# Performance work log

Hardware: AMD Instinct MI355X
Metric: run time of the kernel (lower is better)

Reference implementation:

```python
import jax, jax.numpy as jnp
import numpy as np

N_A, N_B = 30000, 30000
V, D_IN, D_OUT, H, E = 2, 128, 128, 4, 480000
EPS_LN = 1e-5


def setup_inputs() -> dict:
    key = jax.random.key(0)
    ks = jax.random.split(key, 22)
    rn = lambda i, sh, s=1.0: jax.random.normal(ks[i], sh, dtype=jnp.float32) * s
    ri = lambda i, n: jax.random.randint(ks[i], (E,), 0, n, dtype=jnp.int32)
    return {
        'feat_A': rn(0, (N_A, V, D_IN)),
        'feat_B': rn(1, (N_B, V, D_IN)),
        'src_ab': ri(2, N_A), 'dst_ab': ri(3, N_B),
        'val_ab': jax.random.uniform(ks[4], (E,), dtype=jnp.float32),
        'src_ba': ri(5, N_B), 'dst_ba': ri(6, N_A),
        'val_ba': jax.random.uniform(ks[7], (E,), dtype=jnp.float32),
        'W1': rn(8, (D_OUT, D_IN), 0.05), 'b1': jnp.zeros((D_OUT,), jnp.float32),
        'g1': jnp.ones((D_OUT,), jnp.float32), 'be1': jnp.zeros((D_OUT,), jnp.float32),
        'W2': rn(9, (D_OUT, D_IN), 0.05), 'b2': jnp.zeros((D_OUT,), jnp.float32),
        'g2': jnp.ones((D_OUT,), jnp.float32), 'be2': jnp.zeros((D_OUT,), jnp.float32),
        'Win': rn(10, (3 * D_OUT, D_OUT), 0.05), 'bin_': jnp.zeros((3 * D_OUT,), jnp.float32),
        'Wout': rn(11, (D_OUT, D_OUT), 0.05), 'bout': jnp.zeros((D_OUT,), jnp.float32),
        'lng': jnp.ones((D_OUT,), jnp.float32), 'lnb': jnp.zeros((D_OUT,), jnp.float32),
    }


def spmm_t(src, dst, val, h, n_out):
    # (adj^T @ h) over all views: h [N_src, V, d] -> [n_out, V, d]
    msg = h[src] * val[:, None, None]
    return jax.ops.segment_sum(msg, dst, num_segments=n_out)


def l2norm(x):
    n = jnp.sqrt(jnp.sum(x * x, axis=-1, keepdims=True))
    return x / jnp.maximum(n, 1e-12)


def layernorm(x, g, b):
    mu = jnp.mean(x, axis=-1, keepdims=True)
    var = jnp.mean((x - mu) ** 2, axis=-1, keepdims=True)
    return (x - mu) * jax.lax.rsqrt(var + EPS_LN) * g + b


def proj(x, W, b, g, be):
    # Linear -> LayerNorm -> ReLU
    return jax.nn.relu(layernorm(x @ W.T + b, g, be))


def mha(x, Win, bin_, Wout, bout, num_heads):
    # self-attention over the metapath axis P; x [..., P, d]
    *lead, P, d = x.shape
    dh = d // num_heads
    q, k, v = jnp.split(x @ Win.T + bin_, 3, axis=-1)
    hd = lambda t: t.reshape(*lead, P, num_heads, dh)
    q = hd(q) * (dh ** -0.5)
    scores = jnp.einsum('...qhe,...khe->...hqk', q, hd(k))
    a = jax.nn.softmax(scores, axis=-1)
    o = jnp.einsum('...hqk,...khe->...qhe', a, hd(v)).reshape(*lead, P, d)
    return o @ Wout.T + bout


def reference(feat_A, feat_B, src_ab, dst_ab, val_ab, src_ba, dst_ba, val_ba,
              W1, b1, g1, be1, W2, b2, g2, be2, Win, bin_, Wout, bout, lng, lnb):
    # metapath A->B->A
    h = l2norm(spmm_t(src_ab, dst_ab, val_ab, feat_A, N_B))
    h = l2norm(spmm_t(src_ba, dst_ba, val_ba, h, N_A))
    h1 = proj(h, W1, b1, g1, be1)                       # [N_A, V, d]
    # metapath B->A
    h = l2norm(spmm_t(src_ba, dst_ba, val_ba, feat_B, N_A))
    h2 = proj(h, W2, b2, g2, be2)                       # [N_A, V, d]
    x = jnp.stack([h1, h2], axis=2)                     # [N_A, V, P=2, d]
    attn = mha(x, Win, bin_, Wout, bout, H)
    y = layernorm(attn + x, lng, lnb).mean(axis=2)      # [N_A, V, d]
    return y  # h_global['A']; type B is identity passthrough of feat_B
```

## Files before the change

kernel.cpp:

```cpp
#include <hip/hip_runtime.h>

#define D 128
#define NODE_ROW 256
#define AP 8
#define AR (AP * 2)

typedef __attribute__((ext_vector_type(8))) short short8;
typedef __attribute__((ext_vector_type(4))) float floatx4;

__device__ __forceinline__ ushort f2bf(float f) {
    unsigned int u = __float_as_uint(f);
    u += 0x7fffu + ((u >> 16) & 1u);
    return (ushort)(u >> 16);
}
__device__ __forceinline__ unsigned int pk2(float a, float b) {
    return (unsigned int)f2bf(a) | ((unsigned int)f2bf(b) << 16);
}
__device__ __forceinline__ void up8(uint4 u, float* f) {
    f[0] = __uint_as_float(u.x << 16); f[1] = __uint_as_float(u.x & 0xffff0000u);
    f[2] = __uint_as_float(u.y << 16); f[3] = __uint_as_float(u.y & 0xffff0000u);
    f[4] = __uint_as_float(u.z << 16); f[5] = __uint_as_float(u.z & 0xffff0000u);
    f[6] = __uint_as_float(u.w << 16); f[7] = __uint_as_float(u.w & 0xffff0000u);
}
__device__ __forceinline__ float bf2f(ushort h) {
    return __uint_as_float(((unsigned int)h) << 16);
}
__device__ __forceinline__ short8 ldfrag(const ushort* p) {
    union { uint4 u; short8 s; } cv;
    cv.u = *(const uint4*)p;
    return cv.s;
}
__device__ __forceinline__ void acc4(float4& a, float w, uint2 u) {
    a.x += w * __uint_as_float(u.x << 16);
    a.y += w * __uint_as_float(u.x & 0xffff0000u);
    a.z += w * __uint_as_float(u.y << 16);
    a.w += w * __uint_as_float(u.y & 0xffff0000u);
}

__global__ __launch_bounds__(256) void k_f2b2(
    const float* __restrict__ srcA, const float* __restrict__ srcB,
    ushort* __restrict__ dstA, ushort* __restrict__ dstB, int n8) {
    int i = blockIdx.x * 256 + threadIdx.x;
    const float* s; ushort* d; int k;
    if (i < n8) { s = srcA; d = dstA; k = i; }
    else if (i < 2 * n8) { s = srcB; d = dstB; k = i - n8; }
    else return;
    const float4* sp = (const float4*)s + (size_t)k * 2;
    float4 a = sp[0], b = sp[1];
    uint4 o;
    o.x = pk2(a.x, a.y); o.y = pk2(a.z, a.w);
    o.z = pk2(b.x, b.y); o.w = pk2(b.z, b.w);
    ((uint4*)d)[k] = o;
}


__global__ __launch_bounds__(256) void k_hist(
    const int* __restrict__ dst_ab, const int* __restrict__ dst_ba,
    int* __restrict__ cnt_ab, int* __restrict__ cnt_ba, int E) {
    int i = blockIdx.x * 256 + threadIdx.x;
    if (i >= E) return;
    atomicAdd(&cnt_ab[dst_ab[i]], 1);
    atomicAdd(&cnt_ba[dst_ba[i]], 1);
}

__global__ __launch_bounds__(1024) void k_scan(
    const int* __restrict__ cnt, int* __restrict__ start, int n) {
    __shared__ int part[1024];
    int t = threadIdx.x;
    int chunk = (n + 1023) >> 10;
    int lo = min(t * chunk, n), hi = min(lo + chunk, n);
    int s = 0;
    for (int i = lo; i < hi; i++) s += cnt[i];
    part[t] = s;
    __syncthreads();
    for (int d = 1; d < 1024; d <<= 1) {
        int v = (t >= d) ? part[t - d] : 0;
        __syncthreads();
        part[t] += v;
        __syncthreads();
    }
    int off = part[t] - s;
    for (int i = lo; i < hi; i++) { start[i] = off; off += cnt[i]; }
    if (t == 1023) start[n] = off;
}

__global__ __launch_bounds__(256) void k_scatter(
    const int* __restrict__ src_ab, const int* __restrict__ dst_ab,
    const float* __restrict__ val_ab,
    const int* __restrict__ src_ba, const int* __restrict__ dst_ba,
    const float* __restrict__ val_ba,
    const int* __restrict__ start_ab, const int* __restrict__ start_ba,
    int* __restrict__ cnt_ab, int* __restrict__ cnt_ba,
    int2* __restrict__ ep_ab, int2* __restrict__ ep_ba, int E) {
    int i = blockIdx.x * 256 + threadIdx.x;
    if (i >= E) return;
    {
        int dd = dst_ab[i];
        int pos = start_ab[dd] + atomicAdd(&cnt_ab[dd], 1);
        ep_ab[pos] = make_int2(src_ab[i], __float_as_int(val_ab[i]));
    }
    {
        int dd = dst_ba[i];
        int pos = start_ba[dd] + atomicAdd(&cnt_ba[dd], 1);
        ep_ba[pos] = make_int2(src_ba[i], __float_as_int(val_ba[i]));
    }
}


__global__ __launch_bounds__(256) void k_gather_norm_bf(
    const ushort* __restrict__ feat, const int2* __restrict__ ep,
    const int* __restrict__ start, ushort* __restrict__ out, int n) {
    int node = blockIdx.x * 4 + (threadIdx.x >> 6);
    if (node >= n) return;
    int lane = threadIdx.x & 63;
    int lo = start[node], hi = start[node + 1];
    float4 acc = make_float4(0.f, 0.f, 0.f, 0.f);
    int i = lo;
    for (; i + 3 < hi; i += 4) {
        int2 p0 = ep[i], p1 = ep[i + 1], p2 = ep[i + 2], p3 = ep[i + 3];
        uint2 u0 = ((const uint2*)(feat + (size_t)p0.x * NODE_ROW))[lane];
        uint2 u1 = ((const uint2*)(feat + (size_t)p1.x * NODE_ROW))[lane];
        uint2 u2 = ((const uint2*)(feat + (size_t)p2.x * NODE_ROW))[lane];
        uint2 u3 = ((const uint2*)(feat + (size_t)p3.x * NODE_ROW))[lane];
        acc4(acc, __int_as_float(p0.y), u0);
        acc4(acc, __int_as_float(p1.y), u1);
        acc4(acc, __int_as_float(p2.y), u2);
        acc4(acc, __int_as_float(p3.y), u3);
    }
    for (; i < hi; i++) {
        int2 p = ep[i];
        uint2 u = ((const uint2*)(feat + (size_t)p.x * NODE_ROW))[lane];
        acc4(acc, __int_as_float(p.y), u);
    }
    float ss = acc.x * acc.x + acc.y * acc.y + acc.z * acc.z + acc.w * acc.w;
    #pragma unroll
    for (int o = 16; o > 0; o >>= 1) ss += __shfl_xor(ss, o, 32);
    float sc = 1.0f / fmaxf(sqrtf(ss), 1e-12f);
    uint2 o;
    o.x = pk2(acc.x * sc, acc.y * sc);
    o.y = pk2(acc.z * sc, acc.w * sc);
    ((uint2*)(out + (size_t)node * NODE_ROW))[lane] = o;
}

__global__ __launch_bounds__(256) void k_gather2_bf(
    const ushort* __restrict__ featP, const ushort* __restrict__ featQ,
    const int2* __restrict__ ep, const int* __restrict__ start,
    ushort* __restrict__ outP, ushort* __restrict__ outQ, int n) {
    int node = blockIdx.x * 4 + (threadIdx.x >> 6);
    if (node >= n) return;
    int lane = threadIdx.x & 63;
    int lo = start[node], hi = start[node + 1];
    float4 aP = make_float4(0.f, 0.f, 0.f, 0.f);
    float4 aQ = make_float4(0.f, 0.f, 0.f, 0.f);
    int i = lo;
    for (; i + 3 < hi; i += 4) {
        int2 p0 = ep[i], p1 = ep[i + 1], p2 = ep[i + 2], p3 = ep[i + 3];
        size_t o0 = (size_t)p0.x * NODE_ROW, o1 = (size_t)p1.x * NODE_ROW;
        size_t o2 = (size_t)p2.x * NODE_ROW, o3 = (size_t)p3.x * NODE_ROW;
        uint2 uP0 = ((const uint2*)(featP + o0))[lane];
        uint2 uQ0 = ((const uint2*)(featQ + o0))[lane];
        uint2 uP1 = ((const uint2*)(featP + o1))[lane];
        uint2 uQ1 = ((const uint2*)(featQ + o1))[lane];
        uint2 uP2 = ((const uint2*)(featP + o2))[lane];
        uint2 uQ2 = ((const uint2*)(featQ + o2))[lane];
        uint2 uP3 = ((const uint2*)(featP + o3))[lane];
        uint2 uQ3 = ((const uint2*)(featQ + o3))[lane];
        float w0 = __int_as_float(p0.y), w1 = __int_as_float(p1.y);
        float w2 = __int_as_float(p2.y), w3 = __int_as_float(p3.y);
        acc4(aP, w0, uP0); acc4(aQ, w0, uQ0);
        acc4(aP, w1, uP1); acc4(aQ, w1, uQ1);
        acc4(aP, w2, uP2); acc4(aQ, w2, uQ2);
        acc4(aP, w3, uP3); acc4(aQ, w3, uQ3);
    }
    for (; i < hi; i++) {
        int2 p = ep[i];
        float w = __int_as_float(p.y);
        size_t off = (size_t)p.x * NODE_ROW;
        uint2 uP = ((const uint2*)(featP + off))[lane];
        uint2 uQ = ((const uint2*)(featQ + off))[lane];
        acc4(aP, w, uP); acc4(aQ, w, uQ);
    }
    uint2 oP, oQ;
    oP.x = pk2(aP.x, aP.y); oP.y = pk2(aP.z, aP.w);
    oQ.x = pk2(aQ.x, aQ.y); oQ.y = pk2(aQ.z, aQ.w);
    ((uint2*)(outP + (size_t)node * NODE_ROW))[lane] = oP;
    ((uint2*)(outQ + (size_t)node * NODE_ROW))[lane] = oQ;
}

__global__ __launch_bounds__(256) void k_cvt(
    const float* __restrict__ W1, const float* __restrict__ W2,
    const float* __restrict__ Win, const float* __restrict__ Wout,
    ushort* __restrict__ dst) {
    int idx = (blockIdx.x * 256 + threadIdx.x) * 4;
    if (idx >= 98304) return;
    const float* s; int off;
    if (idx < 16384)      { s = W1;  off = idx; }
    else if (idx < 32768) { s = W2;  off = idx - 16384; }
    else if (idx < 81920) { s = Win; off = idx - 32768; }
    else                  { s = Wout; off = idx - 81920; }
    float4 f = *(const float4*)(s + off);
    uint2 p;
    p.x = pk2(f.x, f.y);
    p.y = pk2(f.z, f.w);
    *(uint2*)(dst + idx) = p;
}

__global__ __launch_bounds__(128) void k_projm(
    const ushort* __restrict__ in, const ushort* __restrict__ Wb,
    const float* __restrict__ b, const float* __restrict__ g,
    const float* __restrict__ be, ushort* __restrict__ xbuf, int p) {
    __shared__ ushort xn[16][136];
    __shared__ float yb[16][128];
    int t = threadIdx.x;
    size_t rowbase = (size_t)blockIdx.x * 16;
    int r = t >> 3, i = t & 7;

    {
        const ushort* gp = in + (rowbase + r) * D + i * 16;
        float v[16];
        up8(((const uint4*)gp)[0], v);
        up8(((const uint4*)gp)[1], v + 8);
        float ss = 0.f;
        #pragma unroll
        for (int e = 0; e < 16; e++) ss += v[e] * v[e];
        ss += __shfl_xor(ss, 1, 8);
        ss += __shfl_xor(ss, 2, 8);
        ss += __shfl_xor(ss, 4, 8);
        float sc = 1.0f / fmaxf(sqrtf(ss), 1e-12f);
        uint4 w0, w1;
        w0.x = pk2(v[0]*sc, v[1]*sc);   w0.y = pk2(v[2]*sc, v[3]*sc);
        w0.z = pk2(v[4]*sc, v[5]*sc);   w0.w = pk2(v[6]*sc, v[7]*sc);
        w1.x = pk2(v[8]*sc, v[9]*sc);   w1.y = pk2(v[10]*sc, v[11]*sc);
        w1.z = pk2(v[12]*sc, v[13]*sc); w1.w = pk2(v[14]*sc, v[15]*sc);
        ushort* dst = &xn[r][i * 16];
        ((uint4*)dst)[0] = w0;
        ((uint4*)dst)[1] = w1;
    }
    __syncthreads();

    {
        int lane = t & 63, w = t >> 6, c = lane & 15, quad = lane >> 4;
        short8 af[4];
        #pragma unroll
        for (int kt = 0; kt < 4; kt++)
            af[kt] = ldfrag(&xn[c][kt * 32 + quad * 8]);
        #pragma unroll
        for (int nt2 = 0; nt2 < 4; nt2++) {
            int j = (w * 4 + nt2) * 16 + c;
            floatx4 acc = {0.f, 0.f, 0.f, 0.f};
            #pragma unroll
            for (int kt = 0; kt < 4; kt++) {
                short8 bfr = ldfrag(Wb + (size_t)j * 128 + kt * 32 + quad * 8);
                acc = __builtin_amdgcn_mfma_f32_16x16x32_bf16(af[kt], bfr, acc, 0, 0, 0);
            }
            float bj = b[j];
            #pragma unroll
            for (int rg = 0; rg < 4; rg++)
                yb[quad * 4 + rg][j] = acc[rg] + bj;
        }
    }
    __syncthreads();

    {
        float v[16];
        const float* yr = &yb[r][i * 16];
        #pragma unroll
        for (int e = 0; e < 16; e++) v[e] = yr[e];
        float s1 = 0.f, s2 = 0.f;
        #pragma unroll
        for (int e = 0; e < 16; e++) { s1 += v[e]; s2 += v[e] * v[e]; }
        s1 += __shfl_xor(s1, 1, 8); s2 += __shfl_xor(s2, 1, 8);
        s1 += __shfl_xor(s1, 2, 8); s2 += __shfl_xor(s2, 2, 8);
        s1 += __shfl_xor(s1, 4, 8); s2 += __shfl_xor(s2, 4, 8);
        float mu = s1 * (1.0f / 128.0f);
        float var = s2 * (1.0f / 128.0f) - mu * mu;
        float rs = rsqrtf(var + 1e-5f);
        const float* gg = g + i * 16;
        const float* bb = be + i * 16;
        float res[16];
        #pragma unroll
        for (int e = 0; e < 16; e++)
            res[e] = fmaxf((v[e] - mu) * rs * gg[e] + bb[e], 0.f);
        ushort* op = xbuf + ((rowbase + r) * 2 + p) * D + i * 16;
        uint4 w0, w1;
        w0.x = pk2(res[0], res[1]);   w0.y = pk2(res[2], res[3]);
        w0.z = pk2(res[4], res[5]);   w0.w = pk2(res[6], res[7]);
        w1.x = pk2(res[8], res[9]);   w1.y = pk2(res[10], res[11]);
        w1.z = pk2(res[12], res[13]); w1.w = pk2(res[14], res[15]);
        ((uint4*)op)[0] = w0;
        ((uint4*)op)[1] = w1;
    }
}

__global__ __launch_bounds__(384, 8) void k_attn2(
    const ushort* __restrict__ xbuf,
    const ushort* __restrict__ Winb, const float* __restrict__ binq,
    const ushort* __restrict__ Woutb, const float* __restrict__ bout,
    const float* __restrict__ lng, const float* __restrict__ lnb,
    float* __restrict__ out) {
    __shared__ ushort xb[AR][136];
    __shared__ float qk[AR][256];
    __shared__ ushort vb[AR][136];
    __shared__ ushort ob[AR][136];
    __shared__ float aw[AP][4][2][2];
    __shared__ float mu_s[AR], rs_s[AR];
    int t = threadIdx.x;
    int lane = t & 63, w = t >> 6;
    int c = lane & 15, quad = lane >> 4;
    size_t pairbase = (size_t)blockIdx.x * AP;
    size_t rowbase = pairbase * 2;

    const uint2* gx = (const uint2*)(xbuf + rowbase * D);
    for (int i = t; i < AR * D / 4; i += 384) {
        int r = i >> 5;
        int col = (i & 31) * 4;
        *(uint2*)&xb[r][col] = gx[i];
    }
    __syncthreads();

    {
        short8 af[4];
        #pragma unroll
        for (int kt = 0; kt < 4; kt++)
            af[kt] = ldfrag(&xb[c][kt * 32 + quad * 8]);
        #pragma unroll
        for (int nt2 = 0; nt2 < 4; nt2++) {
            int j = (w * 4 + nt2) * 16 + c;
            floatx4 acc = {0.f, 0.f, 0.f, 0.f};
            #pragma unroll
            for (int kt = 0; kt < 4; kt++) {
                short8 bfr = ldfrag(Winb + (size_t)j * 128 + kt * 32 + quad * 8);
                acc = __builtin_amdgcn_mfma_f32_16x16x32_bf16(af[kt], bfr, acc, 0, 0, 0);
            }
            float bj = binq[j];
            if (j < 256) {
                float sc = (j < 128) ? 0.17677669529663687f : 1.0f;
                #pragma unroll
                for (int rg = 0; rg < 4; rg++)
                    qk[quad * 4 + rg][j] = (acc[rg] + bj) * sc;
            } else {
                #pragma unroll
                for (int rg = 0; rg < 4; rg++)
                    vb[quad * 4 + rg][j - 256] = f2bf(acc[rg] + bj);
            }
        }
    }
    __syncthreads();

    if (t < AP * 4) {
        int pp = t >> 2, h = t & 3;
        int r0 = pp * 2, r1 = r0 + 1;
        const float* q0 = &qk[r0][h * 32];
        const float* q1 = &qk[r1][h * 32];
        const float* k0 = &qk[r0][128 + h * 32];
        const float* k1 = &qk[r1][128 + h * 32];
        float s00 = 0, s01 = 0, s10 = 0, s11 = 0;
        #pragma unroll
        for (int e = 0; e < 32; e++) {
            float a0 = q0[e], a1 = q1[e], c0 = k0[e], c1 = k1[e];
            s00 += a0 * c0; s01 += a0 * c1; s10 += a1 * c0; s11 += a1 * c1;
        }
        float m0 = fmaxf(s00, s01);
        float e00 = __expf(s00 - m0), e01 = __expf(s01 - m0);
        float i0 = 1.f / (e00 + e01);
        aw[pp][h][0][0] = e00 * i0; aw[pp][h][0][1] = e01 * i0;
        float m1 = fmaxf(s10, s11);
        float e10 = __expf(s10 - m1), e11 = __expf(s11 - m1);
        float i1 = 1.f / (e10 + e11);
        aw[pp][h][1][0] = e10 * i1; aw[pp][h][1][1] = e11 * i1;
    }
    __syncthreads();

    for (int q2 = t; q2 < AR * D / 4; q2 += 384) {
        int r = q2 >> 5;
        int col = (q2 & 31) * 4;
        int pp = r >> 1, pq = r & 1, h = col >> 5;
        float a0 = aw[pp][h][pq][0], a1 = aw[pp][h][pq][1];
        uint2 u0 = *(const uint2*)&vb[pp * 2][col];
        uint2 u1 = *(const uint2*)&vb[pp * 2 + 1][col];
        float o0 = a0 * __uint_as_float(u0.x << 16)        + a1 * __uint_as_float(u1.x << 16);
        float o1 = a0 * __uint_as_float(u0.x & 0xffff0000u) + a1 * __uint_as_float(u1.x & 0xffff0000u);
        float o2 = a0 * __uint_as_float(u0.y << 16)        + a1 * __uint_as_float(u1.y << 16);
        float o3 = a0 * __uint_as_float(u0.y & 0xffff0000u) + a1 * __uint_as_float(u1.y & 0xffff0000u);
        uint2 pw;
        pw.x = pk2(o0, o1); pw.y = pk2(o2, o3);
        *(uint2*)&ob[r][col] = pw;
    }
    __syncthreads();

    if (w < 4) {
        short8 af[4];
        #pragma unroll
        for (int kt = 0; kt < 4; kt++)
            af[kt] = ldfrag(&ob[c][kt * 32 + quad * 8]);
        #pragma unroll
        for (int nt2 = 0; nt2 < 2; nt2++) {
            int j = (w * 2 + nt2) * 16 + c;
            floatx4 acc = {0.f, 0.f, 0.f, 0.f};
            #pragma unroll
            for (int kt = 0; kt < 4; kt++) {
                short8 bfr = ldfrag(Woutb + (size_t)j * 128 + kt * 32 + quad * 8);
                acc = __builtin_amdgcn_mfma_f32_16x16x32_bf16(af[kt], bfr, acc, 0, 0, 0);
            }
            float bj = bout[j];
            #pragma unroll
            for (int rg = 0; rg < 4; rg++) {
                int row = quad * 4 + rg;
                qk[row][j] = acc[rg] + bj + bf2f(xb[row][j]);
            }
        }
    }
    __syncthreads();

    if (t < 128) {
        int r = t >> 3, i = t & 7;
        float s1 = 0.f, s2 = 0.f;
        const float* yr = &qk[r][i * 16];
        #pragma unroll
        for (int cc = 0; cc < 16; cc++) { float v = yr[cc]; s1 += v; s2 += v * v; }
        s1 += __shfl_down(s1, 4, 8); s2 += __shfl_down(s2, 4, 8);
        s1 += __shfl_down(s1, 2, 8); s2 += __shfl_down(s2, 2, 8);
        s1 += __shfl_down(s1, 1, 8); s2 += __shfl_down(s2, 1, 8);
        if (i == 0) {
            float mu = s1 / D;
            float var = s2 / D - mu * mu;
            mu_s[r] = mu; rs_s[r] = rsqrtf(var + 1e-5f);
        }
    }
    __syncthreads();

    if (t < 128) {
        int j = t;
        float gj = lng[j], bj = lnb[j];
        #pragma unroll
        for (int pp = 0; pp < AP; pp++) {
            int r0 = pp * 2, r1 = r0 + 1;
            float v0 = (qk[r0][j] - mu_s[r0]) * rs_s[r0] * gj + bj;
            float v1 = (qk[r1][j] - mu_s[r1]) * rs_s[r1] * gj + bj;
            out[(pairbase + pp) * D + j] = 0.5f * (v0 + v1);
        }
    }
}

extern "C" void kernel_launch(void* const* d_in, const int* in_sizes, int n_in,
                              void* d_out, int out_size, void* d_ws, size_t ws_size,
                              hipStream_t stream) {
    const float* feat_A = (const float*)d_in[0];
    const float* feat_B = (const float*)d_in[1];
    const int*   src_ab = (const int*)d_in[2];
    const int*   dst_ab = (const int*)d_in[3];
    const float* val_ab = (const float*)d_in[4];
    const int*   src_ba = (const int*)d_in[5];
    const int*   dst_ba = (const int*)d_in[6];
    const float* val_ba = (const float*)d_in[7];
    const float* W1 = (const float*)d_in[8];
    const float* b1 = (const float*)d_in[9];
    const float* g1 = (const float*)d_in[10];
    const float* be1 = (const float*)d_in[11];
    const float* W2 = (const float*)d_in[12];
    const float* b2 = (const float*)d_in[13];
    const float* g2 = (const float*)d_in[14];
    const float* be2 = (const float*)d_in[15];
    const float* Win = (const float*)d_in[16];
    const float* binq = (const float*)d_in[17];
    const float* Wout = (const float*)d_in[18];
    const float* bout = (const float*)d_in[19];
    const float* lng = (const float*)d_in[20];
    const float* lnb = (const float*)d_in[21];

    int E  = in_sizes[2];
    int nA = in_sizes[0] / NODE_ROW;
    int nB = in_sizes[1] / NODE_ROW;
    int rowsA = nA * 2;
    size_t nodeElems = (size_t)nA * NODE_ROW;

    ushort* fbA  = (ushort*)d_ws;
    ushort* fbB  = fbA + nodeElems;
    ushort* hB   = fbB + nodeElems;
    ushort* hA1  = hB + nodeElems;
    ushort* hA2  = hA1 + nodeElems;
    ushort* xbuf = hA2 + nodeElems;
    ushort* Wbf  = xbuf + (size_t)rowsA * 2 * D;
    ushort* W1b   = Wbf;
    ushort* W2b   = Wbf + 16384;
    ushort* Winb  = Wbf + 32768;
    ushort* Woutb = Wbf + 81920;
    int* cnt_ab   = (int*)(Wbf + 98304);
    int* cnt_ba   = cnt_ab + nB;
    int* start_ab = cnt_ba + nA;
    int* start_ba = start_ab + (nB + 1);
    uintptr_t a = (uintptr_t)(start_ba + (nA + 1));
    a = (a + 15) & ~(uintptr_t)15;
    int2* ep_ab = (int2*)a;
    int2* ep_ba = ep_ab + E;

    int egrid = (E + 255) / 256;
    int n8 = (int)(nodeElems / 8);

    k_f2b2<<<(2 * n8 + 255) / 256, 256, 0, stream>>>(feat_A, feat_B, fbA, fbB, n8);

    hipMemsetAsync(cnt_ab, 0, (size_t)(nA + nB) * sizeof(int), stream);
    k_hist<<<egrid, 256, 0, stream>>>(dst_ab, dst_ba, cnt_ab, cnt_ba, E);
    k_scan<<<1, 1024, 0, stream>>>(cnt_ab, start_ab, nB);
    k_scan<<<1, 1024, 0, stream>>>(cnt_ba, start_ba, nA);
    hipMemsetAsync(cnt_ab, 0, (size_t)(nA + nB) * sizeof(int), stream);
    k_scatter<<<egrid, 256, 0, stream>>>(src_ab, dst_ab, val_ab,
                                         src_ba, dst_ba, val_ba,
                                         start_ab, start_ba, cnt_ab, cnt_ba,
                                         ep_ab, ep_ba, E);

    k_cvt<<<96, 256, 0, stream>>>(W1, W2, Win, Wout, Wbf);

    k_gather_norm_bf<<<(nB + 3) / 4, 256, 0, stream>>>(fbA, ep_ab, start_ab, hB, nB);
    k_gather2_bf<<<(nA + 3) / 4, 256, 0, stream>>>(hB, fbB, ep_ba, start_ba,
                                                   hA1, hA2, nA);

    k_projm<<<rowsA / 16, 128, 0, stream>>>(hA1, W1b, b1, g1, be1, xbuf, 0);
    k_projm<<<rowsA / 16, 128, 0, stream>>>(hA2, W2b, b2, g2, be2, xbuf, 1);
    k_attn2<<<rowsA / AP, 384, 0, stream>>>(xbuf, Winb, binq, Woutb, bout,
                                            lng, lnb, (float*)d_out);
}
```

Measured before the change: 587.8 us.

## Merge two scans into one launch, reuse counts as cursors, fuse attention softmax

The two single-block prefix scans are merged into one two-block launch. The scan now writes exclusive offsets back into the count arrays, so the scatter kernel uses them directly as atomic cursors, which drops a memset and one start-array load per edge. In the attention kernel, the 32-thread score and softmax step and the separate weighted-V pass are merged into a single 256-thread phase that uses shuffles, removing one barrier and the aw shared array. The ordering of edges within each CSR bucket is still nondeterministic, as before.

Result: no change. 580.8 us (-1.2%).

```diff
diff --git a/kernel.cpp b/kernel.cpp
--- a/kernel.cpp
+++ b/kernel.cpp
@@ -63,9 +63,13 @@
     atomicAdd(&cnt_ba[dst_ba[i]], 1);
 }
 
-__global__ __launch_bounds__(1024) void k_scan(
-    const int* __restrict__ cnt, int* __restrict__ start, int n) {
+__global__ __launch_bounds__(1024) void k_scan2(
+    int* __restrict__ cntB, int* __restrict__ startB, int nB_,
+    int* __restrict__ cntA, int* __restrict__ startA, int nA_) {
     __shared__ int part[1024];
+    int* cnt; int* start; int n;
+    if (blockIdx.x == 0) { cnt = cntB; start = startB; n = nB_; }
+    else                 { cnt = cntA; start = startA; n = nA_; }
     int t = threadIdx.x;
     int chunk = (n + 1023) >> 10;
     int lo = min(t * chunk, n), hi = min(lo + chunk, n);
@@ -80,7 +84,12 @@
         __syncthreads();
     }
     int off = part[t] - s;
-    for (int i = lo; i < hi; i++) { start[i] = off; off += cnt[i]; }
+    for (int i = lo; i < hi; i++) {
+        int c = cnt[i];
+        start[i] = off;
+        cnt[i] = off;
+        off += c;
+    }
     if (t == 1023) start[n] = off;
 }
 
@@ -89,19 +98,16 @@
     const float* __restrict__ val_ab,
     const int* __restrict__ src_ba, const int* __restrict__ dst_ba,
     const float* __restrict__ val_ba,
-    const int* __restrict__ start_ab, const int* __restrict__ start_ba,
-    int* __restrict__ cnt_ab, int* __restrict__ cnt_ba,
+    int* __restrict__ cur_ab, int* __restrict__ cur_ba,
     int2* __restrict__ ep_ab, int2* __restrict__ ep_ba, int E) {
     int i = blockIdx.x * 256 + threadIdx.x;
     if (i >= E) return;
     {
-        int dd = dst_ab[i];
-        int pos = start_ab[dd] + atomicAdd(&cnt_ab[dd], 1);
+        int pos = atomicAdd(&cur_ab[dst_ab[i]], 1);
         ep_ab[pos] = make_int2(src_ab[i], __float_as_int(val_ab[i]));
     }
     {
-        int dd = dst_ba[i];
-        int pos = start_ba[dd] + atomicAdd(&cnt_ba[dd], 1);
+        int pos = atomicAdd(&cur_ba[dst_ba[i]], 1);
         ep_ba[pos] = make_int2(src_ba[i], __float_as_int(val_ba[i]));
     }
 }
@@ -302,7 +308,6 @@
     __shared__ float qk[AR][256];
     __shared__ ushort vb[AR][136];
     __shared__ ushort ob[AR][136];
-    __shared__ float aw[AP][4][2][2];
     __shared__ float mu_s[AR], rs_s[AR];
     int t = threadIdx.x;
     int lane = t & 63, w = t >> 6;
@@ -347,44 +352,41 @@
     }
     __syncthreads();
 
-    if (t < AP * 4) {
-        int pp = t >> 2, h = t & 3;
-        int r0 = pp * 2, r1 = r0 + 1;
-        const float* q0 = &qk[r0][h * 32];
-        const float* q1 = &qk[r1][h * 32];
-        const float* k0 = &qk[r0][128 + h * 32];
-        const float* k1 = &qk[r1][128 + h * 32];
-        float s00 = 0, s01 = 0, s10 = 0, s11 = 0;
-        #pragma unroll
-        for (int e = 0; e < 32; e++) {
-            float a0 = q0[e], a1 = q1[e], c0 = k0[e], c1 = k1[e];
-            s00 += a0 * c0; s01 += a0 * c1; s10 += a1 * c0; s11 += a1 * c1;
-        }
-        float m0 = fmaxf(s00, s01);
-        float e00 = __expf(s00 - m0), e01 = __expf(s01 - m0);
-        float i0 = 1.f / (e00 + e01);
-        aw[pp][h][0][0] = e00 * i0; aw[pp][h][0][1] = e01 * i0;
-        float m1 = fmaxf(s10, s11);
-        float e10 = __expf(s10 - m1), e11 = __expf(s11 - m1);
-        float i1 = 1.f / (e10 + e11);
-        aw[pp][h][1][0] = e10 * i1; aw[pp][h][1][1] = e11 * i1;
-    }
-    __syncthreads();
-
-    for (int q2 = t; q2 < AR * D / 4; q2 += 384) {
-        int r = q2 >> 5;
-        int col = (q2 & 31) * 4;
-        int pp = r >> 1, pq = r & 1, h = col >> 5;
-        float a0 = aw[pp][h][pq][0], a1 = aw[pp][h][pq][1];
-        uint2 u0 = *(const uint2*)&vb[pp * 2][col];
-        uint2 u1 = *(const uint2*)&vb[pp * 2 + 1][col];
-        float o0 = a0 * __uint_as_float(u0.x << 16)        + a1 * __uint_as_float(u1.x << 16);
-        float o1 = a0 * __uint_as_float(u0.x & 0xffff0000u) + a1 * __uint_as_float(u1.x & 0xffff0000u);
-        float o2 = a0 * __uint_as_float(u0.y << 16)        + a1 * __uint_as_float(u1.y << 16);
-        float o3 = a0 * __uint_as_float(u0.y & 0xffff0000u) + a1 * __uint_as_float(u1.y & 0xffff0000u);
-        uint2 pw;
-        pw.x = pk2(o0, o1); pw.y = pk2(o2, o3);
-        *(uint2*)&ob[r][col] = pw;
+    if (t < 256) {
+        int half = t & 1, kk = (t >> 1) & 1, pq = (t >> 2) & 1;
+        int h = (t >> 3) & 3, pp = t >> 5;
+        int qrow = 2 * pp + pq;
+        const float4* qp = (const float4*)&qk[qrow][h * 32 + half * 16];
+        const float4* kp = (const float4*)&qk[2 * pp + kk][128 + h * 32 + half * 16];
+        float s = 0.f;
+        #pragma unroll
+        for (int m = 0; m < 4; m++) {
+            float4 qv = qp[m], kv = kp[m];
+            s += qv.x * kv.x + qv.y * kv.y + qv.z * kv.z + qv.w * kv.w;
+        }
+        s += __shfl_xor(s, 1, 64);
+        float so = __shfl_xor(s, 2, 64);
+        float s0 = kk ? so : s;
+        float s1 = kk ? s : so;
+        float m0 = fmaxf(s0, s1);
+        float e0 = __expf(s0 - m0), e1 = __expf(s1 - m0);
+        float inv = 1.f / (e0 + e1);
+        float a0 = e0 * inv, a1 = e1 * inv;
+        int cbase = h * 32 + kk * 16 + half * 8;
+        const uint2* v0p = (const uint2*)&vb[2 * pp][cbase];
+        const uint2* v1p = (const uint2*)&vb[2 * pp + 1][cbase];
+        ushort* op = &ob[qrow][cbase];
+        #pragma unroll
+        for (int m = 0; m < 2; m++) {
+            uint2 u0 = v0p[m], u1 = v1p[m];
+            float o0 = a0 * __uint_as_float(u0.x << 16)         + a1 * __uint_as_float(u1.x << 16);
+            float o1 = a0 * __uint_as_float(u0.x & 0xffff0000u) + a1 * __uint_as_float(u1.x & 0xffff0000u);
+            float o2 = a0 * __uint_as_float(u0.y << 16)         + a1 * __uint_as_float(u1.y << 16);
+            float o3 = a0 * __uint_as_float(u0.y & 0xffff0000u) + a1 * __uint_as_float(u1.y & 0xffff0000u);
+            uint2 pw;
+            pw.x = pk2(o0, o1); pw.y = pk2(o2, o3);
+            ((uint2*)op)[m] = pw;
+        }
     }
     __syncthreads();
 
@@ -501,13 +503,10 @@
 
     hipMemsetAsync(cnt_ab, 0, (size_t)(nA + nB) * sizeof(int), stream);
     k_hist<<<egrid, 256, 0, stream>>>(dst_ab, dst_ba, cnt_ab, cnt_ba, E);
-    k_scan<<<1, 1024, 0, stream>>>(cnt_ab, start_ab, nB);
-    k_scan<<<1, 1024, 0, stream>>>(cnt_ba, start_ba, nA);
-    hipMemsetAsync(cnt_ab, 0, (size_t)(nA + nB) * sizeof(int), stream);
+    k_scan2<<<2, 1024, 0, stream>>>(cnt_ab, start_ab, nB, cnt_ba, start_ba, nA);
     k_scatter<<<egrid, 256, 0, stream>>>(src_ab, dst_ab, val_ab,
                                          src_ba, dst_ba, val_ba,
-                                         start_ab, start_ba, cnt_ab, cnt_ba,
-                                         ep_ab, ep_ba, E);
+                                         cnt_ab, cnt_ba, ep_ab, ep_ba, E);
 
     k_cvt<<<96, 256, 0, stream>>>(W1, W2, Win, Wout, Wbf);
 
```
